# Kernel tuning notes

Measured on AMD Instinct MI355X. Metric: run time of the kernel, lower is better.

## Reference

```python
import jax, jax.numpy as jnp
import numpy as np

C1 = 256
C2 = 256
C = 256

def setup_inputs() -> dict:
    key = jax.random.key(0)
    ks = jax.random.split(key, 8)
    B, S, H, W = 4, 8, 32, 32
    img_feat = jax.random.normal(ks[0], (B, S, C1, H, W), dtype=jnp.float32)
    depth_feat = jax.random.normal(ks[1], (B, S, C2, H, W), dtype=jnp.float32)
    sq = 1.0 / np.sqrt(C1)
    sk = 1.0 / np.sqrt(C2)
    Wq = jax.random.uniform(ks[2], (C1, C), jnp.float32, -sq, sq)
    bq = jax.random.uniform(ks[3], (C,), jnp.float32, -sq, sq)
    Wk = jax.random.uniform(ks[4], (C2, C), jnp.float32, -sk, sk)
    bk = jax.random.uniform(ks[5], (C,), jnp.float32, -sk, sk)
    Wv = jax.random.uniform(ks[6], (C2, C), jnp.float32, -sk, sk)
    bv = jax.random.uniform(ks[7], (C,), jnp.float32, -sk, sk)
    return {"img_feat": img_feat, "depth_feat": depth_feat,
            "Wq": Wq, "bq": bq, "Wk": Wk, "bk": bk, "Wv": Wv, "bv": bv}

def reference(img_feat, depth_feat, Wq, bq, Wk, bk, Wv, bv):
    B, S, _, H, W = img_feat.shape
    hw = H * W
    # channels-last, flatten spatial: [B,S,hw,c1]
    img = jnp.transpose(img_feat, (0, 1, 3, 4, 2)).reshape(B, S, hw, -1)
    depth = jnp.transpose(depth_feat, (0, 1, 3, 4, 2)).reshape(B, S, hw, -1)
    q = (img @ Wq + bq).astype(jnp.float32)    # [B,S,hw,c]
    k = (depth @ Wk + bk).astype(jnp.float32)  # [B,S,hw,c]
    v = (depth @ Wv + bv).astype(jnp.float32)  # [B,S,hw,c]
    scale = 1.0 / jnp.sqrt(jnp.float32(Wq.shape[1]))
    scores = jnp.einsum('bsqc,bskc->bsqk', q, k) * scale  # [B,S,hw,hw]
    attn = jax.nn.softmax(scores, axis=-1)
    out = jnp.einsum('bsqk,bskc->bsqc', attn, v)          # [B,S,hw,c]
    out = out + img                                        # residual (c == c1)
    out = out.reshape(B, S, H, W, -1).astype(img_feat.dtype)
    return jnp.transpose(out, (0, 1, 4, 2, 3))             # [B,S,c,H,W]
```

## Files before the change

kernel.cpp:

```cpp
#include <hip/hip_runtime.h>
#include <hip/hip_bf16.h>

typedef __hip_bfloat16 bf16;
typedef __attribute__((ext_vector_type(8))) short short8v;
typedef __attribute__((ext_vector_type(4))) float f32x4;

#define NSLICE 32
#define HW     1024
#define CDIM   256
#define KVT    32

__global__ __launch_bounds__(256)
void wt_prep_kernel(const float* __restrict__ Wq, const float* __restrict__ Wk,
                    const float* __restrict__ Wv, bf16* __restrict__ wt)
{
    const int m = blockIdx.x >> 8;
    const int r = blockIdx.x & 255;
    const int tid = threadIdx.x;
    const float* W = (m == 0) ? Wq : (m == 1) ? Wk : Wv;
    const float sc = (m == 0) ? 0.0625f : 1.0f;
    wt[((size_t)m << 16) + (size_t)tid * 256 + r] = __float2bfloat16(W[r * 256 + tid] * sc);
}

__global__ __launch_bounds__(256)
void proj_q_kernel(const float* __restrict__ img, const bf16* __restrict__ wt,
                   const float* __restrict__ bq, bf16* __restrict__ qo)
{
    const int bid   = blockIdx.x;
    const int s     = (bid & 7) * 4 + ((bid >> 3) & 3);
    const int tt    = (bid >> 5) & 15;
    const int chalf = bid >> 9;
    const int t0    = tt * 64;

    const int tid  = threadIdx.x;
    const int wave = tid >> 6;
    const int lane = tid & 63;
    const int lo16 = lane & 15;
    const int hi4  = lane >> 4;
    const int cw0  = chalf * 128 + wave * 32;

    __shared__ short Ai[64][40];

    const int so = tid >> 6, st = tid & 63;
    const float* imgS = img + (size_t)s * CDIM * HW + t0;

    f32x4 aq[2][4];
    #pragma unroll
    for (int a = 0; a < 2; ++a)
        #pragma unroll
        for (int b = 0; b < 4; ++b) aq[a][b] = (f32x4){0.f, 0.f, 0.f, 0.f};

    float ri[8];
    #pragma unroll
    for (int j = 0; j < 8; ++j) ri[j] = imgS[(size_t)(so * 8 + j) * HW + st];

    for (int kc = 0; kc < 8; ++kc) {
        __syncthreads();
        {
            short ti[8];
            #pragma unroll
            for (int j = 0; j < 8; ++j) {
                bf16 hb = __float2bfloat16(ri[j]);
                ti[j] = *reinterpret_cast<short*>(&hb);
            }
            *reinterpret_cast<short8v*>(&Ai[st][so * 8]) = *reinterpret_cast<short8v*>(ti);
        }
        __syncthreads();

        if (kc < 7) {
            #pragma unroll
            for (int j = 0; j < 8; ++j)
                ri[j] = imgS[(size_t)((kc + 1) * 32 + so * 8 + j) * HW + st];
        }

        short8v xi[4];
        #pragma unroll
        for (int nf = 0; nf < 4; ++nf)
            xi[nf] = *reinterpret_cast<const short8v*>(&Ai[nf * 16 + lo16][hi4 * 8]);

        const int koff = kc * 32 + hi4 * 8;
        short8v wqf[2];
        #pragma unroll
        for (int mf = 0; mf < 2; ++mf)
            wqf[mf] = *reinterpret_cast<const short8v*>(
                wt + (size_t)(cw0 + mf * 16 + lo16) * 256 + koff);

        #pragma unroll
        for (int mf = 0; mf < 2; ++mf)
            #pragma unroll
            for (int nf = 0; nf < 4; ++nf)
                aq[mf][nf] = __builtin_amdgcn_mfma_f32_16x16x32_bf16(wqf[mf], xi[nf], aq[mf][nf], 0, 0, 0);
    }

    #pragma unroll
    for (int mf = 0; mf < 2; ++mf) {
        const int cb = cw0 + mf * 16 + 4 * hi4;
        const float4 b4 = *reinterpret_cast<const float4*>(bq + cb);
        const float ba[4] = {b4.x * 0.0625f, b4.y * 0.0625f, b4.z * 0.0625f, b4.w * 0.0625f};
        #pragma unroll
        for (int nf = 0; nf < 4; ++nf) {
            const int tok = t0 + nf * 16 + lo16;
            bf16 tq[4];
            #pragma unroll
            for (int g = 0; g < 4; ++g)
                tq[g] = __float2bfloat16(aq[mf][nf][g] + ba[g]);
            *reinterpret_cast<uint2*>(&qo[((size_t)s * HW + tok) * CDIM + cb]) =
                *reinterpret_cast<uint2*>(tq);
        }
    }
}

__global__ __launch_bounds__(256)
void proj_kv_kernel(const float* __restrict__ dep, const bf16* __restrict__ wt,
                    const float* __restrict__ bk, const float* __restrict__ bv,
                    bf16* __restrict__ ko, bf16* __restrict__ vt)
{
    const int bid   = blockIdx.x;
    const int s     = (bid & 7) * 4 + ((bid >> 3) & 3);
    const int tt    = (bid >> 5) & 15;
    const int chalf = bid >> 9;
    const int t0    = tt * 64;

    const int tid  = threadIdx.x;
    const int wave = tid >> 6;
    const int lane = tid & 63;
    const int lo16 = lane & 15;
    const int hi4  = lane >> 4;
    const int cw0  = chalf * 128 + wave * 32;

    __shared__ short Ad[64][40];

    const int so = tid >> 6, st = tid & 63;
    const float* depS = dep + (size_t)s * CDIM * HW + t0;
    const bf16* wtk = wt + (1 << 16);
    const bf16* wtv = wt + (2 << 16);

    f32x4 ak[2][4], av[4][2];
    #pragma unroll
    for (int a = 0; a < 2; ++a)
        #pragma unroll
        for (int b = 0; b < 4; ++b) {
            ak[a][b] = (f32x4){0.f, 0.f, 0.f, 0.f};
            av[b][a] = (f32x4){0.f, 0.f, 0.f, 0.f};
        }

    float rd[8];
    #pragma unroll
    for (int j = 0; j < 8; ++j) rd[j] = depS[(size_t)(so * 8 + j) * HW + st];

    for (int kc = 0; kc < 8; ++kc) {
        __syncthreads();
        {
            short td[8];
            #pragma unroll
            for (int j = 0; j < 8; ++j) {
                bf16 hb = __float2bfloat16(rd[j]);
                td[j] = *reinterpret_cast<short*>(&hb);
            }
            *reinterpret_cast<short8v*>(&Ad[st][so * 8]) = *reinterpret_cast<short8v*>(td);
        }
        __syncthreads();

        if (kc < 7) {
            #pragma unroll
            for (int j = 0; j < 8; ++j)
                rd[j] = depS[(size_t)((kc + 1) * 32 + so * 8 + j) * HW + st];
        }

        short8v xd[4];
        #pragma unroll
        for (int nf = 0; nf < 4; ++nf)
            xd[nf] = *reinterpret_cast<const short8v*>(&Ad[nf * 16 + lo16][hi4 * 8]);

        const int koff = kc * 32 + hi4 * 8;
        short8v wkf[2], wvf[2];
        #pragma unroll
        for (int mf = 0; mf < 2; ++mf) {
            const size_t wrow = (size_t)(cw0 + mf * 16 + lo16) * 256 + koff;
            wkf[mf] = *reinterpret_cast<const short8v*>(wtk + wrow);
            wvf[mf] = *reinterpret_cast<const short8v*>(wtv + wrow);
        }

        #pragma unroll
        for (int mf = 0; mf < 2; ++mf)
            #pragma unroll
            for (int nf = 0; nf < 4; ++nf)
                ak[mf][nf] = __builtin_amdgcn_mfma_f32_16x16x32_bf16(wkf[mf], xd[nf], ak[mf][nf], 0, 0, 0);
        #pragma unroll
        for (int mf = 0; mf < 4; ++mf)
            #pragma unroll
            for (int nf = 0; nf < 2; ++nf)
                av[mf][nf] = __builtin_amdgcn_mfma_f32_16x16x32_bf16(xd[mf], wvf[nf], av[mf][nf], 0, 0, 0);
    }

    #pragma unroll
    for (int mf = 0; mf < 2; ++mf) {
        const int cb = cw0 + mf * 16 + 4 * hi4;
        const float4 b4 = *reinterpret_cast<const float4*>(bk + cb);
        const float ba[4] = {b4.x, b4.y, b4.z, b4.w};
        #pragma unroll
        for (int nf = 0; nf < 4; ++nf) {
            const int tok = t0 + nf * 16 + lo16;
            bf16 tk[4];
            #pragma unroll
            for (int g = 0; g < 4; ++g)
                tk[g] = __float2bfloat16(ak[mf][nf][g] + ba[g]);
            *reinterpret_cast<uint2*>(&ko[((size_t)s * HW + tok) * CDIM + cb]) =
                *reinterpret_cast<uint2*>(tk);
        }
    }
    #pragma unroll
    for (int nf = 0; nf < 2; ++nf) {
        const int c = cw0 + nf * 16 + lo16;
        const float bvv = bv[c];
        #pragma unroll
        for (int mf = 0; mf < 4; ++mf) {
            const int tb = t0 + mf * 16 + 4 * hi4;
            bf16 tv[4];
            #pragma unroll
            for (int g = 0; g < 4; ++g)
                tv[g] = __float2bfloat16(av[mf][nf][g] + bvv);
            *reinterpret_cast<uint2*>(&vt[((size_t)s * CDIM + c) * HW + tb]) =
                *reinterpret_cast<uint2*>(tv);
        }
    }
}

__global__ __launch_bounds__(256)
void flash_mfma_kernel(const bf16* __restrict__ q, const bf16* __restrict__ k,
                       const bf16* __restrict__ vt, const float* __restrict__ img,
                       float* __restrict__ out)
{
    const int bid = blockIdx.x;
    const int s   = (bid & 7) * 4 + ((bid >> 3) & 3);
    const int t0  = (bid >> 5) * 128;

    const int tid  = threadIdx.x;
    const int wave = tid >> 6;
    const int lane = tid & 63;
    const int lo16 = lane & 15;
    const int hi4  = lane >> 4;

    __shared__ short KsL[32 * 256];
    __shared__ short VsL[256 * 32];
    __shared__ short PsL[4 * 2 * 512];

    const int rowbase = t0 + wave * 32;

    short8v qf[2][8];
    #pragma unroll
    for (int m = 0; m < 2; ++m) {
        const bf16* qp = q + ((size_t)s * HW + rowbase + m * 16 + lo16) * CDIM + hi4 * 8;
        #pragma unroll
        for (int kf = 0; kf < 8; ++kf)
            qf[m][kf] = *reinterpret_cast<const short8v*>(qp + kf * 32);
    }

    f32x4 Oa[16], Ob[16];
    #pragma unroll
    for (int cf = 0; cf < 16; ++cf) {
        Oa[cf] = (f32x4){0.f, 0.f, 0.f, 0.f};
        Ob[cf] = (f32x4){0.f, 0.f, 0.f, 0.f};
    }
    float lp[2][4] = {{0.f, 0.f, 0.f, 0.f}, {0.f, 0.f, 0.f, 0.f}};

    const bf16* kS  = k  + (size_t)s * HW * CDIM;
    const bf16* vtS = vt + (size_t)s * CDIM * HW;

    const int krow = tid >> 3;
    const int kch  = tid & 7;
    const int kxor = krow & 7;
    const int vxor = (tid >> 1) & 3;

    short8v kreg[4], vreg[4];
    #pragma unroll
    for (int u = 0; u < 4; ++u) {
        kreg[u] = *reinterpret_cast<const short8v*>(kS + (size_t)krow * CDIM + (kch + 8 * u) * 8);
        vreg[u] = *reinterpret_cast<const short8v*>(vtS + (size_t)tid * HW + u * 8);
    }

    const int pvRow = lo16 * 32 + (hi4 ^ ((lo16 >> 1) & 3)) * 8;
    for (int kt = 0; kt < HW / KVT; ++kt) {
        __syncthreads();
        #pragma unroll
        for (int u = 0; u < 4; ++u)
            *reinterpret_cast<short8v*>(&KsL[krow * 256 + ((kch ^ kxor) + 8 * u) * 8]) = kreg[u];
        #pragma unroll
        for (int u = 0; u < 4; ++u)
            *reinterpret_cast<short8v*>(&VsL[tid * 32 + (u ^ vxor) * 8]) = vreg[u];
        __syncthreads();

        if (kt + 1 < HW / KVT) {
            const bf16* src = kS + (size_t)(kt + 1) * KVT * CDIM;
            #pragma unroll
            for (int u = 0; u < 4; ++u) {
                kreg[u] = *reinterpret_cast<const short8v*>(src + (size_t)krow * CDIM + (kch + 8 * u) * 8);
                vreg[u] = *reinterpret_cast<const short8v*>(vtS + (size_t)tid * HW + (kt + 1) * KVT + u * 8);
            }
        }

        f32x4 sa[2][2];
        sa[0][0] = (f32x4){0.f, 0.f, 0.f, 0.f};
        sa[0][1] = (f32x4){0.f, 0.f, 0.f, 0.f};
        sa[1][0] = (f32x4){0.f, 0.f, 0.f, 0.f};
        sa[1][1] = (f32x4){0.f, 0.f, 0.f, 0.f};
        __builtin_amdgcn_s_setprio(1);
        #pragma unroll
        for (int ks = 0; ks < 8; ++ks) {
            #pragma unroll
            for (int cf = 0; cf < 2; ++cf) {
                const int row = cf * 16 + lo16;
                const short8v bfr = *reinterpret_cast<const short8v*>(
                    &KsL[row * 256 + ((4 * ks + hi4) ^ (lo16 & 7)) * 8]);
                sa[0][cf] = __builtin_amdgcn_mfma_f32_16x16x32_bf16(qf[0][ks], bfr, sa[0][cf], 0, 0, 0);
                sa[1][cf] = __builtin_amdgcn_mfma_f32_16x16x32_bf16(qf[1][ks], bfr, sa[1][cf], 0, 0, 0);
            }
        }
        __builtin_amdgcn_s_setprio(0);

        #pragma unroll
        for (int m = 0; m < 2; ++m)
            #pragma unroll
            for (int cf = 0; cf < 2; ++cf)
                #pragma unroll
                for (int g = 0; g < 4; ++g) {
                    const float e = __expf(sa[m][cf][g]);
                    lp[m][g] += e;
                    bf16 hb = __float2bfloat16(e);
                    const int r = 4 * hi4 + g;
                    const int ch = (2 * cf + (lo16 >> 3)) ^ ((r >> 1) & 3);
                    PsL[wave * 1024 + m * 512 + r * 32 + ch * 8 + (lo16 & 7)] =
                        *reinterpret_cast<short*>(&hb);
                }

        const short8v pa0 = *reinterpret_cast<const short8v*>(&PsL[wave * 1024 + pvRow]);
        const short8v pa1 = *reinterpret_cast<const short8v*>(&PsL[wave * 1024 + 512 + pvRow]);

        __builtin_amdgcn_s_setprio(1);
        #pragma unroll
        for (int cf = 0; cf < 16; ++cf) {
            const int row = cf * 16 + lo16;
            const short8v vb = *reinterpret_cast<const short8v*>(
                &VsL[row * 32 + (hi4 ^ ((lo16 >> 1) & 3)) * 8]);
            Oa[cf] = __builtin_amdgcn_mfma_f32_16x16x32_bf16(pa0, vb, Oa[cf], 0, 0, 0);
            Ob[cf] = __builtin_amdgcn_mfma_f32_16x16x32_bf16(pa1, vb, Ob[cf], 0, 0, 0);
        }
        __builtin_amdgcn_s_setprio(0);
    }

    const float* imgS = img + (size_t)s * CDIM * HW;
    float*       outS = out + (size_t)s * CDIM * HW;
    #pragma unroll
    for (int m = 0; m < 2; ++m) {
        float inv[4];
        #pragma unroll
        for (int g = 0; g < 4; ++g) {
            float l = lp[m][g];
            #pragma unroll
            for (int off = 1; off < 16; off <<= 1) l += __shfl_xor(l, off);
            inv[g] = 1.0f / l;
        }
        const int tt = rowbase + m * 16 + 4 * hi4;
        #pragma unroll
        for (int cf = 0; cf < 16; ++cf) {
            const int c = cf * 16 + lo16;
            const f32x4 O = (m == 0) ? Oa[cf] : Ob[cf];
            const float4 r4 = *reinterpret_cast<const float4*>(imgS + (size_t)c * HW + tt);
            float4 o;
            o.x = O[0] * inv[0] + r4.x;
            o.y = O[1] * inv[1] + r4.y;
            o.z = O[2] * inv[2] + r4.z;
            o.w = O[3] * inv[3] + r4.w;
            *reinterpret_cast<float4*>(outS + (size_t)c * HW + tt) = o;
        }
    }
}

extern "C" void kernel_launch(void* const* d_in, const int* in_sizes, int n_in,
                              void* d_out, int out_size, void* d_ws, size_t ws_size,
                              hipStream_t stream)
{
    const float* img = (const float*)d_in[0];
    const float* dep = (const float*)d_in[1];
    const float* Wq  = (const float*)d_in[2];
    const float* bq  = (const float*)d_in[3];
    const float* Wk  = (const float*)d_in[4];
    const float* bk  = (const float*)d_in[5];
    const float* Wv  = (const float*)d_in[6];
    const float* bv  = (const float*)d_in[7];
    float* out = (float*)d_out;

    const size_t npt  = (size_t)NSLICE * HW * CDIM;
    const size_t need = 3 * npt * sizeof(bf16) + 3 * 65536 * sizeof(bf16);
    if (ws_size < need) {
        hipMemsetAsync(d_out, 0, (size_t)out_size * sizeof(float), stream);
        return;
    }

    bf16* q  = (bf16*)d_ws;
    bf16* k  = q + npt;
    bf16* vt = k + npt;
    bf16* wt = vt + npt;

    wt_prep_kernel<<<dim3(3 * 256), 256, 0, stream>>>(Wq, Wk, Wv, wt);

    proj_q_kernel<<<dim3(NSLICE * 32), 256, 0, stream>>>(img, wt, bq, q);
    proj_kv_kernel<<<dim3(NSLICE * 32), 256, 0, stream>>>(dep, wt, bk, bv, k, vt);

    flash_mfma_kernel<<<dim3(NSLICE * 8), 256, 0, stream>>>(q, k, vt, img, out);
}
```

Measured before the change: 132.5 us.

## Split attention KV range across two blocks and merge partials in combine kernel

When the workspace is large enough, the flash kernel launches twice as many blocks, and each block handles half of the key/value tiles for its query tile. Each half writes its unnormalized partial output and row sums: one half to the output buffer in fp32, the other to a bf16 scratch buffer. A new combine kernel adds the two partials, divides by the summed row sums and adds the residual. This aims to raise CU occupancy over the original one-block-per-CU grid, at the cost of an extra kernel launch, extra global traffic for the partials and some precision loss from storing one partial in bf16.

```diff
diff --git a/kernel.cpp b/kernel.cpp
--- a/kernel.cpp
+++ b/kernel.cpp
@@ -229,11 +229,24 @@
 __global__ __launch_bounds__(256)
 void flash_mfma_kernel(const bf16* __restrict__ q, const bf16* __restrict__ k,
                        const bf16* __restrict__ vt, const float* __restrict__ img,
-                       float* __restrict__ out)
+                       float* __restrict__ out, float* __restrict__ l0,
+                       float* __restrict__ l1, bf16* __restrict__ part1,
+                       int split)
 {
     const int bid = blockIdx.x;
     const int s   = (bid & 7) * 4 + ((bid >> 3) & 3);
-    const int t0  = (bid >> 5) * 128;
+    int qt, kt0, kt1, mode;
+    if (split) {
+        const int half = (bid >> 5) & 1;
+        qt  = bid >> 6;
+        kt0 = half * 16;
+        kt1 = kt0 + 16;
+        mode = 1 + half;
+    } else {
+        qt = bid >> 5;
+        kt0 = 0; kt1 = 32; mode = 0;
+    }
+    const int t0 = qt * 128;
 
     const int tid  = threadIdx.x;
     const int wave = tid >> 6;
@@ -275,12 +288,14 @@
     short8v kreg[4], vreg[4];
     #pragma unroll
     for (int u = 0; u < 4; ++u) {
-        kreg[u] = *reinterpret_cast<const short8v*>(kS + (size_t)krow * CDIM + (kch + 8 * u) * 8);
-        vreg[u] = *reinterpret_cast<const short8v*>(vtS + (size_t)tid * HW + u * 8);
+        kreg[u] = *reinterpret_cast<const short8v*>(
+            kS + (size_t)(kt0 * KVT + krow) * CDIM + (kch + 8 * u) * 8);
+        vreg[u] = *reinterpret_cast<const short8v*>(
+            vtS + (size_t)tid * HW + kt0 * KVT + u * 8);
     }
 
     const int pvRow = lo16 * 32 + (hi4 ^ ((lo16 >> 1) & 3)) * 8;
-    for (int kt = 0; kt < HW / KVT; ++kt) {
+    for (int kt = kt0; kt < kt1; ++kt) {
         __syncthreads();
         #pragma unroll
         for (int u = 0; u < 4; ++u)
@@ -290,7 +305,7 @@
             *reinterpret_cast<short8v*>(&VsL[tid * 32 + (u ^ vxor) * 8]) = vreg[u];
         __syncthreads();
 
-        if (kt + 1 < HW / KVT) {
+        if (kt + 1 < kt1) {
             const bf16* src = kS + (size_t)(kt + 1) * KVT * CDIM;
             #pragma unroll
             for (int u = 0; u < 4; ++u) {
@@ -352,28 +367,94 @@
     float*       outS = out + (size_t)s * CDIM * HW;
     #pragma unroll
     for (int m = 0; m < 2; ++m) {
-        float inv[4];
+        float lred[4];
         #pragma unroll
         for (int g = 0; g < 4; ++g) {
             float l = lp[m][g];
             #pragma unroll
             for (int off = 1; off < 16; off <<= 1) l += __shfl_xor(l, off);
-            inv[g] = 1.0f / l;
+            lred[g] = l;
         }
         const int tt = rowbase + m * 16 + 4 * hi4;
-        #pragma unroll
-        for (int cf = 0; cf < 16; ++cf) {
-            const int c = cf * 16 + lo16;
-            const f32x4 O = (m == 0) ? Oa[cf] : Ob[cf];
-            const float4 r4 = *reinterpret_cast<const float4*>(imgS + (size_t)c * HW + tt);
-            float4 o;
-            o.x = O[0] * inv[0] + r4.x;
-            o.y = O[1] * inv[1] + r4.y;
-            o.z = O[2] * inv[2] + r4.z;
-            o.w = O[3] * inv[3] + r4.w;
-            *reinterpret_cast<float4*>(outS + (size_t)c * HW + tt) = o;
-        }
-    }
+
+        if (mode == 0) {
+            float inv[4];
+            #pragma unroll
+            for (int g = 0; g < 4; ++g) inv[g] = 1.0f / lred[g];
+            #pragma unroll
+            for (int cf = 0; cf < 16; ++cf) {
+                const int c = cf * 16 + lo16;
+                const f32x4 O = (m == 0) ? Oa[cf] : Ob[cf];
+                const float4 r4 = *reinterpret_cast<const float4*>(imgS + (size_t)c * HW + tt);
+                float4 o;
+                o.x = O[0] * inv[0] + r4.x;
+                o.y = O[1] * inv[1] + r4.y;
+                o.z = O[2] * inv[2] + r4.z;
+                o.w = O[3] * inv[3] + r4.w;
+                *reinterpret_cast<float4*>(outS + (size_t)c * HW + tt) = o;
+            }
+        } else if (mode == 1) {
+            if (lo16 == 0) {
+                #pragma unroll
+                for (int g = 0; g < 4; ++g) l0[s * HW + tt + g] = lred[g];
+            }
+            #pragma unroll
+            for (int cf = 0; cf < 16; ++cf) {
+                const int c = cf * 16 + lo16;
+                const f32x4 O = (m == 0) ? Oa[cf] : Ob[cf];
+                float4 o = {O[0], O[1], O[2], O[3]};
+                *reinterpret_cast<float4*>(outS + (size_t)c * HW + tt) = o;
+            }
+        } else {
+            if (lo16 == 0) {
+                #pragma unroll
+                for (int g = 0; g < 4; ++g) l1[s * HW + tt + g] = lred[g];
+            }
+            bf16* pS = part1 + (size_t)s * CDIM * HW;
+            #pragma unroll
+            for (int cf = 0; cf < 16; ++cf) {
+                const int c = cf * 16 + lo16;
+                const f32x4 O = (m == 0) ? Oa[cf] : Ob[cf];
+                bf16 t4[4];
+                #pragma unroll
+                for (int g = 0; g < 4; ++g) t4[g] = __float2bfloat16(O[g]);
+                *reinterpret_cast<uint2*>(pS + (size_t)c * HW + tt) =
+                    *reinterpret_cast<uint2*>(t4);
+            }
+        }
+    }
+}
+
+__global__ __launch_bounds__(256)
+void combine_kernel(const float* __restrict__ img, const bf16* __restrict__ part1,
+                    const float* __restrict__ l0, const float* __restrict__ l1,
+                    float* __restrict__ out)
+{
+    const int bid = blockIdx.x;
+    const int s   = (bid & 7) * 4 + ((bid >> 3) & 3);
+    const int c   = bid >> 5;
+    const int t   = threadIdx.x * 4;
+
+    const size_t base = ((size_t)s * CDIM + c) * HW + t;
+    const float4 o0 = *reinterpret_cast<const float4*>(out + base);
+    const uint2 p1r = *reinterpret_cast<const uint2*>(part1 + base);
+    const unsigned short* pu = (const unsigned short*)&p1r;
+    const float4 L0 = *reinterpret_cast<const float4*>(l0 + s * HW + t);
+    const float4 L1 = *reinterpret_cast<const float4*>(l1 + s * HW + t);
+    const float4 r4 = *reinterpret_cast<const float4*>(img + base);
+
+    float p1f[4];
+    #pragma unroll
+    for (int j = 0; j < 4; ++j) {
+        unsigned int u = ((unsigned int)pu[j]) << 16;
+        p1f[j] = *reinterpret_cast<float*>(&u);
+    }
+    float4 o;
+    o.x = (o0.x + p1f[0]) / (L0.x + L1.x) + r4.x;
+    o.y = (o0.y + p1f[1]) / (L0.y + L1.y) + r4.y;
+    o.z = (o0.z + p1f[2]) / (L0.z + L1.z) + r4.z;
+    o.w = (o0.w + p1f[3]) / (L0.w + L1.w) + r4.w;
+    *reinterpret_cast<float4*>(out + base) = o;
 }
 
 extern "C" void kernel_launch(void* const* d_in, const int* in_sizes, int n_in,
@@ -390,22 +471,35 @@
     const float* bv  = (const float*)d_in[7];
     float* out = (float*)d_out;
 
-    const size_t npt  = (size_t)NSLICE * HW * CDIM;
-    const size_t need = 3 * npt * sizeof(bf16) + 3 * 65536 * sizeof(bf16);
-    if (ws_size < need) {
+    const size_t npt = (size_t)NSLICE * HW * CDIM;
+    const size_t base_need  = 3 * npt * sizeof(bf16) + 3 * 65536 * sizeof(bf16);
+    const size_t split_need = base_need + 2 * (size_t)NSLICE * HW * sizeof(float)
+                            + npt * sizeof(bf16);
+    if (ws_size < base_need) {
         hipMemsetAsync(d_out, 0, (size_t)out_size * sizeof(float), stream);
         return;
     }
+    const int split = (ws_size >= split_need) ? 1 : 0;
 
     bf16* q  = (bf16*)d_ws;
     bf16* k  = q + npt;
     bf16* vt = k + npt;
     bf16* wt = vt + npt;
+    float* l0 = (float*)(wt + 3 * 65536);
+    float* l1 = l0 + (size_t)NSLICE * HW;
+    bf16* part1 = (bf16*)(l1 + (size_t)NSLICE * HW);
 
     wt_prep_kernel<<<dim3(3 * 256), 256, 0, stream>>>(Wq, Wk, Wv, wt);
 
     proj_q_kernel<<<dim3(NSLICE * 32), 256, 0, stream>>>(img, wt, bq, q);
     proj_kv_kernel<<<dim3(NSLICE * 32), 256, 0, stream>>>(dep, wt, bk, bv, k, vt);
 
-    flash_mfma_kernel<<<dim3(NSLICE * 8), 256, 0, stream>>>(q, k, vt, img, out);
+    if (split) {
+        flash_mfma_kernel<<<dim3(NSLICE * 16), 256, 0, stream>>>(
+            q, k, vt, img, out, l0, l1, part1, 1);
+        combine_kernel<<<dim3(NSLICE * CDIM), 256, 0, stream>>>(img, part1, l0, l1, out);
+    } else {
+        flash_mfma_kernel<<<dim3(NSLICE * 8), 256, 0, stream>>>(
+            q, k, vt, img, out, l0, l1, part1, 0);
+    }
 }
```

Result: slower. 152.8 us (+15.3%).
